# Kernel tuning notes

Measured on AMD Instinct MI355X. Metric: run time of the kernel, lower is better.

The kernel has to match this reference:

```python
import jax, jax.numpy as jnp
import numpy as np

EPS = 1e-7
C_CONST = 1.0


def gru_scan(x_seq, h0, Wih, Whh, bih, bhh):
    # x_seq: [T,B,E], h0: [B,H]; torch GRU gate order: r, z, n
    xg = jnp.einsum('tbe,ge->tbg', x_seq, Wih) + bih  # [T,B,3H]

    def step(h, xg_t):
        hg = h @ Whh.T + bhh
        xr, xz, xn = jnp.split(xg_t, 3, axis=-1)
        hr, hz, hn = jnp.split(hg, 3, axis=-1)
        r = jax.nn.sigmoid(xr + hr)
        z = jax.nn.sigmoid(xz + hz)
        n = jnp.tanh(xn + r * hn)
        h_new = (1.0 - z) * n + z * h
        return h_new, h_new

    hT, outs = jax.lax.scan(step, h0, xg)
    return outs, hT


def e2lorentz(x):
    # Euclidean -> Lorentz: [..., D] -> [..., D+1]
    rr = jnp.linalg.norm(x, axis=-1, keepdims=True)
    unit = x / rr
    return jnp.concatenate([unit * jnp.sinh(rr), jnp.cosh(rr)], axis=-1)


def arcosh(x):
    return jnp.log(x) + jnp.log1p(jnp.sqrt(x * x - 1.0 + EPS) / x)


def setup_inputs() -> dict:
    key = jax.random.key(0)
    ks = jax.random.split(key, 14)
    T, B, E, H, V = 64, 1024, 300, 256, 50000
    s = 0.05
    inp = {}
    inp['tokens'] = jax.random.randint(ks[0], (T, B), 0, V, dtype=jnp.int32)
    inp['hidden_state'] = jnp.zeros((2, B, H), jnp.float32)
    inp['emb'] = jax.random.normal(ks[1], (V, E), jnp.float32) * s
    inp['Wih_f'] = jax.random.normal(ks[2], (3 * H, E), jnp.float32) * s
    inp['Whh_f'] = jax.random.normal(ks[3], (3 * H, H), jnp.float32) * s
    inp['bih_f'] = jax.random.normal(ks[4], (3 * H,), jnp.float32) * s
    inp['bhh_f'] = jax.random.normal(ks[5], (3 * H,), jnp.float32) * s
    inp['Wih_b'] = jax.random.normal(ks[6], (3 * H, E), jnp.float32) * s
    inp['Whh_b'] = jax.random.normal(ks[7], (3 * H, H), jnp.float32) * s
    inp['bih_b'] = jax.random.normal(ks[8], (3 * H,), jnp.float32) * s
    inp['bhh_b'] = jax.random.normal(ks[9], (3 * H,), jnp.float32) * s
    inp['attn_W'] = jax.random.normal(ks[10], (2 * H, 2 * H), jnp.float32) * s
    inp['attn_b'] = jax.random.normal(ks[11], (2 * H,), jnp.float32) * s
    inp['centroid'] = jax.random.normal(ks[12], (2 * H,), jnp.float32) * s
    inp['beta'] = jax.random.normal(ks[13], (1,), jnp.float32) * s
    return inp


def reference(tokens, hidden_state, emb, Wih_f, Whh_f, bih_f, bhh_f,
              Wih_b, Whh_b, bih_b, bhh_b, attn_W, attn_b, centroid, beta):
    x = emb[tokens]  # [T,B,E]
    f_fwd, h_f = gru_scan(x, hidden_state[0], Wih_f, Whh_f, bih_f, bhh_f)
    f_bwd_rev, h_b = gru_scan(x[::-1], hidden_state[1], Wih_b, Whh_b, bih_b, bhh_b)
    f_bwd = f_bwd_rev[::-1]
    f_output = jnp.concatenate([f_fwd, f_bwd], axis=-1)  # [T,B,2H]
    h_output = jnp.stack([h_f, h_b], axis=0)             # [2,B,H]

    # hyperbolic attention scores
    a = jnp.tanh(jnp.einsum('tbd,od->tbo', f_output, attn_W) + attn_b)
    aL = e2lorentz(a)                      # [T,B,2H+1]
    uL = e2lorentz(centroid[None, None, :])  # [1,1,2H+1]
    m = aL * uL
    prod = jnp.clip(-jnp.sum(m[..., :-1], axis=-1) + m[..., -1], 1.0 + EPS, 1e16)
    dist = arcosh(prod)                    # [T,B]
    score = -beta[0] * dist - C_CONST
    score = score - score.max()
    alpha = jax.nn.softmax(score, axis=0)  # softmax over time

    # Klein-model features with Lorentz-factor (gamma) weighted midpoint
    fL = e2lorentz(f_output)
    fK = fL[..., :-1] / jnp.clip(fL[..., -1:], EPS, 1e16)  # [T,B,2H]
    dump = jnp.sqrt(jnp.clip(1.0 - jnp.sum(fK * fK, axis=-1), EPS, 1.0 - EPS))
    gamma = jnp.clip(1.0 / dump, 1.0 + EPS, 1e16)
    alpha = alpha * gamma
    alpha = alpha / jnp.sum(alpha, axis=0)
    out = jnp.sum(alpha[..., None] * fK, axis=0)[None]  # [1,B,2H]
    return out, h_output
```

## Files before the change

kernel.cpp:

```cpp
#include <hip/hip_runtime.h>
#include <hip/hip_bf16.h>
#include <math.h>

#define T_  64
#define B_  1024
#define E_  300
#define EP_ 320
#define H_  256
#define G3_ 768
#define D_  512
#define CH_ 16

typedef float f32x4 __attribute__((ext_vector_type(4)));
typedef short bf16x8 __attribute__((ext_vector_type(8)));
typedef unsigned short u16x4 __attribute__((ext_vector_type(4)));

__device__ __forceinline__ float bf2f(unsigned short u){ return __uint_as_float(((unsigned)u) << 16); }
__device__ __forceinline__ unsigned short f2bf(float x){
    __hip_bfloat16 h = __float2bfloat16(x);
    return *(unsigned short*)&h;
}
__device__ __forceinline__ float fsig(float x){ return 1.0f/(1.0f + __expf(-x)); }
__device__ __forceinline__ float ftanh(float x){ return 2.0f/(1.0f + __expf(-2.0f*x)) - 1.0f; }

__global__ void lorentz_u_kernel(const float* __restrict__ centroid,
                                 float* __restrict__ su)
{
    __shared__ float red[512];
    const int tid = threadIdx.x;
    float c = centroid[tid];
    red[tid] = c*c;
    __syncthreads();
    for (int s = 256; s > 0; s >>= 1){
        if (tid < s) red[tid] += red[tid + s];
        __syncthreads();
    }
    float rr = sqrtf(red[0]);
    su[tid] = c / rr * sinhf(rr);
    if (tid == 0) su[512] = coshf(rr);
}

__global__ void cast_pad_kernel(const float* __restrict__ src,
                                __hip_bfloat16* __restrict__ dst,
                                int ncols, int ncols_pad)
{
    long long r = blockIdx.x;
    int c = threadIdx.x;
    float v = (c < ncols) ? src[r*ncols + c] : 0.f;
    dst[r*ncols_pad + c] = __float2bfloat16(v);
}

__global__ void prep_bias_kernel(const float* __restrict__ bihf, const float* __restrict__ bhhf,
                                 const float* __restrict__ bihb, const float* __restrict__ bhhb,
                                 float* __restrict__ biasc)
{
    int c = threadIdx.x, d = blockIdx.x;
    const float* bih = d ? bihb : bihf;
    const float* bhh = d ? bhhb : bhhf;
    biasc[d*G3_ + c] = bih[c] + (c < 2*H_ ? bhh[c] : 0.f);
}

__global__ __launch_bounds__(256) void proj_kernel(
    const int* __restrict__ tokens, int tlo_f, int tlo_b,
    const __hip_bfloat16* __restrict__ embbf,
    const __hip_bfloat16* __restrict__ wihf, const __hip_bfloat16* __restrict__ wihb,
    const float* __restrict__ biasc,
    __hip_bfloat16* __restrict__ xgf, __hip_bfloat16* __restrict__ xgb)
{
    __shared__ char As[64 * 640];
    __shared__ char Ws[64 * 640];
    const int dir = blockIdx.z;
    const int tlo = dir ? tlo_b : tlo_f;
    const __hip_bfloat16* Wbf = dir ? wihb : wihf;
    const float* bias = biasc + dir*G3_;
    __hip_bfloat16* xg = dir ? xgb : xgf;
    const int* tok = tokens + (long long)tlo * B_;

    const int tid = threadIdx.x;
    const int n0 = blockIdx.x * 64;
    const int m0 = blockIdx.y * 64;

    {
        int row = tid >> 2, sub = tid & 3;
        long long tk = tok[m0 + row];
        const char* src = (const char*)(embbf + tk * EP_);
        char* dst = As + row * 640;
        int xm = (row & 7);
        #pragma unroll
        for (int j = 0; j < 10; ++j){
            int slot = sub + j*4;
            float4 v = *(const float4*)(src + slot*16);
            *(float4*)(dst + ((slot ^ xm) * 16)) = v;
        }
    }
    {
        #pragma unroll
        for (int it = 0; it < 10; ++it){
            int idx = it*256 + tid;
            int col = idx / 40, u = idx - col*40;
            float4 v = *(const float4*)(Wbf + (size_t)(n0 + col)*EP_ + u*8);
            *(float4*)(Ws + col*640 + ((u ^ (col & 7)) * 16)) = v;
        }
    }
    __syncthreads();

    const int lane = tid & 63, w = tid >> 6;
    const int arow = w*16 + (lane & 15);
    const int g = lane >> 4, l15 = lane & 15;
    const char* abase = As + arow * 640;
    const int amask = arow & 7;

    f32x4 acc[4];
    #pragma unroll
    for (int i = 0; i < 4; ++i) acc[i] = (f32x4){0.f,0.f,0.f,0.f};

    #pragma unroll
    for (int kc = 0; kc < 10; ++kc){
        int aslot = kc*4 + g;
        bf16x8 a = *(const bf16x8*)(abase + ((aslot ^ amask) * 16));
        #pragma unroll
        for (int ct = 0; ct < 4; ++ct){
            int cl = ct*16 + l15;
            bf16x8 b = *(const bf16x8*)(Ws + cl*640 + ((aslot ^ (cl & 7)) * 16));
            acc[ct] = __builtin_amdgcn_mfma_f32_16x16x32_bf16(a, b, acc[ct], 0, 0, 0);
        }
    }

    #pragma unroll
    for (int ct = 0; ct < 4; ++ct){
        int col = n0 + ct*16 + l15;
        float bv = bias[col];
        int rbase = m0 + w*16 + g*4;
        #pragma unroll
        for (int i = 0; i < 4; ++i)
            xg[(long long)(rbase + i)*G3_ + col] = __float2bfloat16(acc[ct][i] + bv);
    }
}

__global__ __launch_bounds__(512, 1) void gru_chunk_kernel(
    const __hip_bfloat16* __restrict__ xg_f, const __hip_bfloat16* __restrict__ xg_b,
    int tlo_f, int tlo_b,
    __hip_bfloat16* __restrict__ f_bf,
    float* __restrict__ hf32g,
    const float* __restrict__ hidden,
    const __hip_bfloat16* __restrict__ whhbf,
    const float* __restrict__ bhh_f, const float* __restrict__ bhh_b,
    float* __restrict__ hout, int s0)
{
    __shared__ char hlds[2][16 * 512];
    __shared__ char xlds[2][16 * 1536];
    __shared__ float blds[256];
    const int bid = blockIdx.x;
    const int dir = bid & 1;
    const int b0 = (bid >> 1) * 16;
    const int tid = threadIdx.x;
    const int lane = tid & 63, w = tid >> 6;
    const int g = lane >> 4, l15 = lane & 15;
    const int jq = w*32 + g*4;

    const __hip_bfloat16* xg = dir ? xg_b : xg_f;
    const int tlo = dir ? tlo_b : tlo_f;
    const float* bhh = dir ? bhh_b : bhh_f;
    const __hip_bfloat16* Wb = whhbf + (size_t)dir * G3_ * H_;
    float* hfg = hf32g + (size_t)dir * B_ * H_;
    const int b = b0 + l15;

    bf16x8 Wf[3][2][8];
    #pragma unroll
    for (int gate = 0; gate < 3; ++gate)
        #pragma unroll
        for (int tl = 0; tl < 2; ++tl)
            #pragma unroll
            for (int kc = 0; kc < 8; ++kc)
                Wf[gate][tl][kc] = *(const bf16x8*)(Wb +
                    ((size_t)(gate*H_ + w*32 + tl*16 + l15))*H_ + kc*32 + g*8);

    if (tid < 256) blds[tid] = bhh[2*H_ + tid];

    const float* hsrc = (s0 == 0 ? hidden : hf32g) + (size_t)dir * B_ * H_;
    #pragma unroll
    for (int it = 0; it < 2; ++it){
        int idx = it*512 + tid;
        int r = idx >> 6, q = idx & 63;
        float4 v = *(const float4*)(hsrc + ((size_t)(b0 + r))*H_ + q*4);
        unsigned short t4[4] = { f2bf(v.x), f2bf(v.y), f2bf(v.z), f2bf(v.w) };
        *(uint2*)(hlds[0] + r*512 + (((q>>1) ^ (r&7))*16) + (q&1)*8) = *(uint2*)t4;
    }
    f32x4 carry[2];
    #pragma unroll
    for (int tl = 0; tl < 2; ++tl)
        carry[tl] = *(const f32x4*)&hsrc[(size_t)b*H_ + jq + tl*16];

    auto stage_x = [&](char* dst, const __hip_bfloat16* xgt){
        #pragma unroll
        for (int i = 0; i < 3; ++i){
            int U = (i*8 + w)*64 + lane;
            int r = U / 96;
            int sbase = U - r*96;
            int usrc = sbase - r; if (usrc < 0) usrc += 96;
            const char* src = (const char*)xgt + (size_t)(b0 + r)*1536 + usrc*16;
            __builtin_amdgcn_global_load_lds(
                (const __attribute__((address_space(1))) void*)src,
                (__attribute__((address_space(3))) void*)(dst + (i*8 + w)*1024),
                16, 0, 0);
        }
    };
    {
        const int t0 = dir ? (63 - s0) : s0;
        stage_x(xlds[0], xg + (size_t)(t0 - tlo)*B_*G3_);
    }
    __syncthreads();

    int cur = 0, hc = 0;
    for (int s = s0; s < s0 + CH_; ++s){
        const int t = dir ? (63 - s) : s;

        if (s < s0 + CH_ - 1){
            const int tn = dir ? (t - 1) : (t + 1);
            stage_x(xlds[cur ^ 1], xg + (size_t)(tn - tlo)*B_*G3_);
        }

        f32x4 acc[3][2];
        #pragma unroll
        for (int gate = 0; gate < 3; ++gate)
            #pragma unroll
            for (int tl = 0; tl < 2; ++tl)
                acc[gate][tl] = (f32x4){0.f,0.f,0.f,0.f};

        {
            bf16x8 hb[4];
            #pragma unroll
            for (int kc = 0; kc < 4; ++kc)
                hb[kc] = *(const bf16x8*)(hlds[hc] + l15*512 + (((kc*4 + g) ^ (l15&7))*16));
            #pragma unroll
            for (int kc = 0; kc < 4; ++kc)
                #pragma unroll
                for (int gate = 0; gate < 3; ++gate)
                    #pragma unroll
                    for (int tl = 0; tl < 2; ++tl)
                        acc[gate][tl] = __builtin_amdgcn_mfma_f32_16x16x32_bf16(
                            Wf[gate][tl][kc], hb[kc], acc[gate][tl], 0, 0, 0);
        }
        {
            bf16x8 hb[4];
            #pragma unroll
            for (int kc = 0; kc < 4; ++kc)
                hb[kc] = *(const bf16x8*)(hlds[hc] + l15*512 + ((((kc+4)*4 + g) ^ (l15&7))*16));
            #pragma unroll
            for (int kc = 0; kc < 4; ++kc)
                #pragma unroll
                for (int gate = 0; gate < 3; ++gate)
                    #pragma unroll
                    for (int tl = 0; tl < 2; ++tl)
                        acc[gate][tl] = __builtin_amdgcn_mfma_f32_16x16x32_bf16(
                            Wf[gate][tl][kc+4], hb[kc], acc[gate][tl], 0, 0, 0);
        }

        #pragma unroll
        for (int tl = 0; tl < 2; ++tl){
            u16x4 xv[3];
            #pragma unroll
            for (int gate = 0; gate < 3; ++gate){
                int u = gate*32 + w*4 + tl*2 + (g >> 1);
                int sl = u + l15; if (sl >= 96) sl -= 96;
                xv[gate] = *(const u16x4*)(xlds[cur] + l15*1536 + sl*16 + (g & 1)*8);
            }
            f32x4 bhn = *(const f32x4*)&blds[jq + tl*16];

            unsigned short hb4[4];
            float hn4[4];
            #pragma unroll
            for (int i = 0; i < 4; ++i){
                float xr = bf2f(xv[0][i]);
                float xz = bf2f(xv[1][i]);
                float xn = bf2f(xv[2][i]);
                float r_ = fsig(xr + acc[0][tl][i]);
                float z_ = fsig(xz + acc[1][tl][i]);
                float n_ = ftanh(xn + r_*(acc[2][tl][i] + bhn[i]));
                float hnew = (1.f - z_)*n_ + z_*carry[tl][i];
                carry[tl][i] = hnew;
                hn4[i] = hnew;
                hb4[i] = f2bf(hnew);
            }
            int j0 = jq + tl*16;
            int slot = j0 >> 3;
            *(uint2*)(hlds[hc^1] + l15*512 + ((slot ^ (l15&7))*16) + (j0&7)*2) = *(uint2*)hb4;
            *(u16x4*)((char*)f_bf + (((size_t)t*B_ + b)*D_ + dir*H_ + j0)*2) = *(u16x4*)hb4;
            if (s == 63)
                *(float4*)&hout[(size_t)dir*B_*H_ + (size_t)b*H_ + j0] = *(float4*)hn4;
        }

        __syncthreads();
        cur ^= 1; hc ^= 1;
    }

    #pragma unroll
    for (int tl = 0; tl < 2; ++tl)
        *(f32x4*)&hfg[(size_t)b*H_ + jq + tl*16] = carry[tl];
}

__global__ __launch_bounds__(256) void attn_score_kernel(
    const __hip_bfloat16* __restrict__ f_bf, const __hip_bfloat16* __restrict__ Wbf,
    const float* __restrict__ attn_b, const float* __restrict__ su,
    const float* __restrict__ beta, float* __restrict__ score,
    float* __restrict__ rr2)
{
    __shared__ char WL[65536];
    const int tid = threadIdx.x;
    const int lane = tid & 63, w = tid >> 6;
    const int g = lane >> 4, l15 = lane & 15;
    const long long m0 = (long long)blockIdx.x * 64;
    const long long arow = m0 + w*16 + l15;

    bf16x8 a[16];
    const __hip_bfloat16* ap = f_bf + arow*D_;
    #pragma unroll
    for (int kc = 0; kc < 16; ++kc)
        a[kc] = *(const bf16x8*)(ap + kc*32 + g*8);

    {
        float s2 = 0.f;
        #pragma unroll
        for (int kc = 0; kc < 16; ++kc){
            const unsigned short* hb = (const unsigned short*)&a[kc];
            #pragma unroll
            for (int q = 0; q < 8; ++q){ float x = bf2f(hb[q]); s2 += x*x; }
        }
        s2 += __shfl_xor(s2, 16);
        s2 += __shfl_xor(s2, 32);
        if (g == 0) rr2[arow] = s2;
    }

    float pdot[4] = {0,0,0,0}, pa2[4] = {0,0,0,0};

    for (int nc = 0; nc < 8; ++nc){
        {
            const __hip_bfloat16* wsrc = Wbf + (size_t)nc*64*D_;
            #pragma unroll
            for (int it = 0; it < 16; ++it){
                int idx = it*256 + tid;
                int cl = idx >> 6, jj = idx & 63;
                float4 v = *(const float4*)(wsrc + (size_t)cl*D_ + jj*8);
                *(float4*)(WL + (cl*64 + (jj ^ (cl & 7)))*16) = v;
            }
        }
        __syncthreads();

        f32x4 acc[4];
        #pragma unroll
        for (int i = 0; i < 4; ++i) acc[i] = (f32x4){0.f,0.f,0.f,0.f};
        #pragma unroll
        for (int kc = 0; kc < 16; ++kc){
            #pragma unroll
            for (int ct = 0; ct < 4; ++ct){
                int cl = ct*16 + l15;
                bf16x8 b = *(const bf16x8*)(WL + (cl*64 + ((kc*4 + g) ^ (l15 & 7)))*16);
                acc[ct] = __builtin_amdgcn_mfma_f32_16x16x32_bf16(a[kc], b, acc[ct], 0, 0, 0);
            }
        }
        __syncthreads();

        #pragma unroll
        for (int ct = 0; ct < 4; ++ct){
            int col = nc*64 + ct*16 + l15;
            float bc = attn_b[col], sc = su[col];
            #pragma unroll
            for (int i = 0; i < 4; ++i){
                float av = ftanh(acc[ct][i] + bc);
                pdot[i] += av*sc;
                pa2[i]  += av*av;
            }
        }
    }

    #pragma unroll
    for (int m = 1; m < 16; m <<= 1){
        #pragma unroll
        for (int i = 0; i < 4; ++i){
            pdot[i] += __shfl_xor(pdot[i], m);
            pa2[i]  += __shfl_xor(pa2[i],  m);
        }
    }
    if (l15 == 0){
        const float cu = su[512], bb = beta[0];
        #pragma unroll
        for (int i = 0; i < 4; ++i){
            long long row = m0 + w*16 + g*4 + i;
            float ra  = sqrtf(pa2[i]);
            float shc = sinhf(ra)/ra;
            float prod = cu*coshf(ra) - shc*pdot[i];
            prod = fminf(fmaxf(prod, 1.0f + 1e-7f), 1e16f);
            float dist = logf(prod) + log1pf(sqrtf(prod*prod - 1.0f + 1e-7f)/prod);
            score[row] = -bb * dist;
        }
    }
}

__global__ __launch_bounds__(256) void pool_kernel(
    const __hip_bfloat16* __restrict__ f_bf, const float* __restrict__ score,
    const float* __restrict__ rr2, float* __restrict__ out)
{
    __shared__ float wss[64];
    const int tid = threadIdx.x;
    const long long b = blockIdx.x;

    if (tid < 64){
        int t = tid;
        float sc = score[t*B_ + b];
        float mx = sc;
        #pragma unroll
        for (int m = 1; m < 64; m <<= 1) mx = fmaxf(mx, __shfl_xor(mx, m));
        float e = expf(sc - mx);
        float rr = sqrtf(rr2[t*B_ + b]);
        float th = tanhf(rr);
        float omt = 1.0f - th*th;
        omt = fminf(fmaxf(omt, 1e-7f), 1.0f - 1e-7f);
        float gamma = 1.0f / sqrtf(omt);
        gamma = fminf(fmaxf(gamma, 1.0f + 1e-7f), 1e16f);
        float wgt = e * gamma;
        float ssum = wgt;
        #pragma unroll
        for (int m = 1; m < 64; m <<= 1) ssum += __shfl_xor(ssum, m);
        wss[t] = (wgt / ssum) * (th / rr);
    }
    __syncthreads();

    #pragma unroll
    for (int dd = 0; dd < 2; ++dd){
        int d = tid + dd*256;
        float acc = 0.f;
        for (int t = 0; t < 64; ++t)
            acc += wss[t] * __bfloat162float(f_bf[((long long)t*B_ + b)*D_ + d]);
        out[b*D_ + d] = acc;
    }
}

extern "C" void kernel_launch(void* const* d_in, const int* in_sizes, int n_in,
                              void* d_out, int out_size, void* d_ws, size_t ws_size,
                              hipStream_t stream)
{
    const int*   tokens = (const int*)  d_in[0];
    const float* hidden = (const float*)d_in[1];
    const float* emb    = (const float*)d_in[2];
    const float* Wih_f  = (const float*)d_in[3];
    const float* Whh_f  = (const float*)d_in[4];
    const float* bih_f  = (const float*)d_in[5];
    const float* bhh_f  = (const float*)d_in[6];
    const float* Wih_b  = (const float*)d_in[7];
    const float* Whh_b  = (const float*)d_in[8];
    const float* bih_b  = (const float*)d_in[9];
    const float* bhh_b  = (const float*)d_in[10];
    const float* attn_W = (const float*)d_in[11];
    const float* attn_b = (const float*)d_in[12];
    const float* centroid = (const float*)d_in[13];
    const float* beta   = (const float*)d_in[14];

    const int V = in_sizes[2] / E_;

    char* w = (char*)d_ws;
    __hip_bfloat16* f_bf  = (__hip_bfloat16*)w;  w += (size_t)T_*B_*D_*2;
    __hip_bfloat16* xg_f  = (__hip_bfloat16*)w;  w += (size_t)CH_*B_*G3_*2;
    __hip_bfloat16* xg_b  = (__hip_bfloat16*)w;  w += (size_t)CH_*B_*G3_*2;
    float*          hf32g = (float*)w;           w += (size_t)2*B_*H_*4;
    __hip_bfloat16* embbf = (__hip_bfloat16*)w;  w += (size_t)V*EP_*2;
    __hip_bfloat16* wihf  = (__hip_bfloat16*)w;  w += (size_t)G3_*EP_*2;
    __hip_bfloat16* wihb  = (__hip_bfloat16*)w;  w += (size_t)G3_*EP_*2;
    __hip_bfloat16* whhbf = (__hip_bfloat16*)w;  w += (size_t)2*G3_*H_*2;
    __hip_bfloat16* wat   = (__hip_bfloat16*)w;  w += (size_t)D_*D_*2;
    float*          biasc = (float*)w;           w += (size_t)2*G3_*4;
    float*          score = (float*)w;           w += (size_t)T_*B_*4;
    float*          rr2   = (float*)w;           w += (size_t)T_*B_*4;
    float*          su    = (float*)w;           w += 513*4;

    float* out  = (float*)d_out;
    float* hout = out + (long long)B_*D_;

    lorentz_u_kernel<<<1, 512, 0, stream>>>(centroid, su);
    prep_bias_kernel<<<2, G3_, 0, stream>>>(bih_f, bhh_f, bih_b, bhh_b, biasc);
    cast_pad_kernel<<<V,   EP_, 0, stream>>>(emb,    embbf, E_, EP_);
    cast_pad_kernel<<<G3_, EP_, 0, stream>>>(Wih_f,  wihf,  E_, EP_);
    cast_pad_kernel<<<G3_, EP_, 0, stream>>>(Wih_b,  wihb,  E_, EP_);
    cast_pad_kernel<<<G3_, H_,  0, stream>>>(Whh_f,  whhbf,            H_, H_);
    cast_pad_kernel<<<G3_, H_,  0, stream>>>(Whh_b,  whhbf + (size_t)G3_*H_, H_, H_);
    cast_pad_kernel<<<D_,  D_,  0, stream>>>(attn_W, wat,   D_, D_);

    for (int c = 0; c < T_/CH_; ++c){
        int tlo_f = c*CH_;
        int tlo_b = (T_ - CH_) - c*CH_;
        int s0 = c*CH_;
        proj_kernel<<<dim3(12, CH_*16, 2), 256, 0, stream>>>(
            tokens, tlo_f, tlo_b, embbf, wihf, wihb, biasc, xg_f, xg_b);
        gru_chunk_kernel<<<128, 512, 0, stream>>>(
            xg_f, xg_b, tlo_f, tlo_b, f_bf, hf32g, hidden,
            whhbf, bhh_f, bhh_b, hout, s0);
    }

    attn_score_kernel<<<1024, 256, 0, stream>>>(f_bf, wat, attn_b, su, beta, score, rr2);
    pool_kernel<<<1024, 256, 0, stream>>>(f_bf, score, rr2, out);
}
```

Before: 687.4 us.

## Reuse weight tiles across row tiles and batch f_bf stores in pairs

proj_kernel now keeps its Wih tile in LDS and loops over four 64-row token tiles per block, so W is loaded a quarter as often and the grid shrinks. attn_score_kernel processes 128 rows per block with two A register sets sharing each B fragment, halving attn_W staging. gru_chunk_kernel buffers its per-step f_bf output and writes two timesteps together on odd steps. The cost is more registers and longer serial work per block, which lowers parallelism.

Measured after the change: 705.4 us. 2.6% more time.

```diff
diff --git a/kernel.cpp b/kernel.cpp
--- a/kernel.cpp
+++ b/kernel.cpp
@@ -78,21 +78,7 @@
 
     const int tid = threadIdx.x;
     const int n0 = blockIdx.x * 64;
-    const int m0 = blockIdx.y * 64;
-
-    {
-        int row = tid >> 2, sub = tid & 3;
-        long long tk = tok[m0 + row];
-        const char* src = (const char*)(embbf + tk * EP_);
-        char* dst = As + row * 640;
-        int xm = (row & 7);
-        #pragma unroll
-        for (int j = 0; j < 10; ++j){
-            int slot = sub + j*4;
-            float4 v = *(const float4*)(src + slot*16);
-            *(float4*)(dst + ((slot ^ xm) * 16)) = v;
-        }
-    }
+
     {
         #pragma unroll
         for (int it = 0; it < 10; ++it){
@@ -102,38 +88,56 @@
             *(float4*)(Ws + col*640 + ((u ^ (col & 7)) * 16)) = v;
         }
     }
-    __syncthreads();
 
     const int lane = tid & 63, w = tid >> 6;
-    const int arow = w*16 + (lane & 15);
     const int g = lane >> 4, l15 = lane & 15;
+    const int arow = w*16 + l15;
     const char* abase = As + arow * 640;
     const int amask = arow & 7;
 
-    f32x4 acc[4];
-    #pragma unroll
-    for (int i = 0; i < 4; ++i) acc[i] = (f32x4){0.f,0.f,0.f,0.f};
-
-    #pragma unroll
-    for (int kc = 0; kc < 10; ++kc){
-        int aslot = kc*4 + g;
-        bf16x8 a = *(const bf16x8*)(abase + ((aslot ^ amask) * 16));
+    for (int rt = 0; rt < 4; ++rt){
+        const int m0 = (blockIdx.y*4 + rt) * 64;
+        {
+            int row = tid >> 2, sub = tid & 3;
+            long long tk = tok[m0 + row];
+            const char* src = (const char*)(embbf + tk * EP_);
+            char* dst = As + row * 640;
+            int xm = (row & 7);
+            #pragma unroll
+            for (int j = 0; j < 10; ++j){
+                int slot = sub + j*4;
+                float4 v = *(const float4*)(src + slot*16);
+                *(float4*)(dst + ((slot ^ xm) * 16)) = v;
+            }
+        }
+        __syncthreads();
+
+        f32x4 acc[4];
+        #pragma unroll
+        for (int i = 0; i < 4; ++i) acc[i] = (f32x4){0.f,0.f,0.f,0.f};
+
+        #pragma unroll
+        for (int kc = 0; kc < 10; ++kc){
+            int aslot = kc*4 + g;
+            bf16x8 a = *(const bf16x8*)(abase + ((aslot ^ amask) * 16));
+            #pragma unroll
+            for (int ct = 0; ct < 4; ++ct){
+                int cl = ct*16 + l15;
+                bf16x8 b = *(const bf16x8*)(Ws + cl*640 + ((aslot ^ (cl & 7)) * 16));
+                acc[ct] = __builtin_amdgcn_mfma_f32_16x16x32_bf16(a, b, acc[ct], 0, 0, 0);
+            }
+        }
+
         #pragma unroll
         for (int ct = 0; ct < 4; ++ct){
-            int cl = ct*16 + l15;
-            bf16x8 b = *(const bf16x8*)(Ws + cl*640 + ((aslot ^ (cl & 7)) * 16));
-            acc[ct] = __builtin_amdgcn_mfma_f32_16x16x32_bf16(a, b, acc[ct], 0, 0, 0);
-        }
-    }
-
-    #pragma unroll
-    for (int ct = 0; ct < 4; ++ct){
-        int col = n0 + ct*16 + l15;
-        float bv = bias[col];
-        int rbase = m0 + w*16 + g*4;
-        #pragma unroll
-        for (int i = 0; i < 4; ++i)
-            xg[(long long)(rbase + i)*G3_ + col] = __float2bfloat16(acc[ct][i] + bv);
+            int col = n0 + ct*16 + l15;
+            float bv = bias[col];
+            int rbase = m0 + w*16 + g*4;
+            #pragma unroll
+            for (int i = 0; i < 4; ++i)
+                xg[(long long)(rbase + i)*G3_ + col] = __float2bfloat16(acc[ct][i] + bv);
+        }
+        __syncthreads();
     }
 }
 
@@ -212,6 +216,8 @@
     __syncthreads();
 
     int cur = 0, hc = 0;
+    u16x4 pend[2];
+    int t_pend = -1;
     for (int s = s0; s < s0 + CH_; ++s){
         const int t = dir ? (63 - s) : s;
 
@@ -256,6 +262,7 @@
                             Wf[gate][tl][kc+4], hb[kc], acc[gate][tl], 0, 0, 0);
         }
 
+        u16x4 outv[2];
         #pragma unroll
         for (int tl = 0; tl < 2; ++tl){
             u16x4 xv[3];
@@ -285,9 +292,24 @@
             int j0 = jq + tl*16;
             int slot = j0 >> 3;
             *(uint2*)(hlds[hc^1] + l15*512 + ((slot ^ (l15&7))*16) + (j0&7)*2) = *(uint2*)hb4;
-            *(u16x4*)((char*)f_bf + (((size_t)t*B_ + b)*D_ + dir*H_ + j0)*2) = *(u16x4*)hb4;
+            outv[tl] = *(u16x4*)hb4;
             if (s == 63)
                 *(float4*)&hout[(size_t)dir*B_*H_ + (size_t)b*H_ + j0] = *(float4*)hn4;
+        }
+
+        if (s & 1){
+            if (t_pend >= 0){
+                #pragma unroll
+                for (int tl = 0; tl < 2; ++tl)
+                    *(u16x4*)((char*)f_bf + (((size_t)t_pend*B_ + b)*D_ + dir*H_ + jq + tl*16)*2) = pend[tl];
+            }
+            #pragma unroll
+            for (int tl = 0; tl < 2; ++tl)
+                *(u16x4*)((char*)f_bf + (((size_t)t*B_ + b)*D_ + dir*H_ + jq + tl*16)*2) = outv[tl];
+            t_pend = -1;
+        } else {
+            pend[0] = outv[0]; pend[1] = outv[1];
+            t_pend = t;
         }
 
         __syncthreads();
@@ -309,29 +331,32 @@
     const int tid = threadIdx.x;
     const int lane = tid & 63, w = tid >> 6;
     const int g = lane >> 4, l15 = lane & 15;
-    const long long m0 = (long long)blockIdx.x * 64;
-    const long long arow = m0 + w*16 + l15;
-
-    bf16x8 a[16];
-    const __hip_bfloat16* ap = f_bf + arow*D_;
-    #pragma unroll
-    for (int kc = 0; kc < 16; ++kc)
-        a[kc] = *(const bf16x8*)(ap + kc*32 + g*8);
-
-    {
+    const long long m0 = (long long)blockIdx.x * 128;
+
+    bf16x8 a[2][16];
+    #pragma unroll
+    for (int rg = 0; rg < 2; ++rg){
+        const __hip_bfloat16* ap = f_bf + (m0 + rg*64 + w*16 + l15)*D_;
+        #pragma unroll
+        for (int kc = 0; kc < 16; ++kc)
+            a[rg][kc] = *(const bf16x8*)(ap + kc*32 + g*8);
+    }
+
+    #pragma unroll
+    for (int rg = 0; rg < 2; ++rg){
         float s2 = 0.f;
         #pragma unroll
         for (int kc = 0; kc < 16; ++kc){
-            const unsigned short* hb = (const unsigned short*)&a[kc];
+            const unsigned short* hb = (const unsigned short*)&a[rg][kc];
             #pragma unroll
             for (int q = 0; q < 8; ++q){ float x = bf2f(hb[q]); s2 += x*x; }
         }
         s2 += __shfl_xor(s2, 16);
         s2 += __shfl_xor(s2, 32);
-        if (g == 0) rr2[arow] = s2;
-    }
-
-    float pdot[4] = {0,0,0,0}, pa2[4] = {0,0,0,0};
+        if (g == 0) rr2[m0 + rg*64 + w*16 + l15] = s2;
+    }
+
+    float pdot[2][4] = {}, pa2[2][4] = {};
 
     for (int nc = 0; nc < 8; ++nc){
         {
@@ -346,16 +371,19 @@
         }
         __syncthreads();
 
-        f32x4 acc[4];
-        #pragma unroll
-        for (int i = 0; i < 4; ++i) acc[i] = (f32x4){0.f,0.f,0.f,0.f};
+        f32x4 acc[2][4];
+        #pragma unroll
+        for (int rg = 0; rg < 2; ++rg)
+            #pragma unroll
+            for (int i = 0; i < 4; ++i) acc[rg][i] = (f32x4){0.f,0.f,0.f,0.f};
         #pragma unroll
         for (int kc = 0; kc < 16; ++kc){
             #pragma unroll
             for (int ct = 0; ct < 4; ++ct){
                 int cl = ct*16 + l15;
-                bf16x8 b = *(const bf16x8*)(WL + (cl*64 + ((kc*4 + g) ^ (l15 & 7)))*16);
-                acc[ct] = __builtin_amdgcn_mfma_f32_16x16x32_bf16(a[kc], b, acc[ct], 0, 0, 0);
+                bf16x8 bfr = *(const bf16x8*)(WL + (cl*64 + ((kc*4 + g) ^ (l15 & 7)))*16);
+                acc[0][ct] = __builtin_amdgcn_mfma_f32_16x16x32_bf16(a[0][kc], bfr, acc[0][ct], 0, 0, 0);
+                acc[1][ct] = __builtin_amdgcn_mfma_f32_16x16x32_bf16(a[1][kc], bfr, acc[1][ct], 0, 0, 0);
             }
         }
         __syncthreads();
@@ -365,33 +393,41 @@
             int col = nc*64 + ct*16 + l15;
             float bc = attn_b[col], sc = su[col];
             #pragma unroll
+            for (int rg = 0; rg < 2; ++rg){
+                #pragma unroll
+                for (int i = 0; i < 4; ++i){
+                    float av = ftanh(acc[rg][ct][i] + bc);
+                    pdot[rg][i] += av*sc;
+                    pa2[rg][i]  += av*av;
+                }
+            }
+        }
+    }
+
+    #pragma unroll
+    for (int m = 1; m < 16; m <<= 1){
+        #pragma unroll
+        for (int rg = 0; rg < 2; ++rg)
+            #pragma unroll
             for (int i = 0; i < 4; ++i){
-                float av = ftanh(acc[ct][i] + bc);
-                pdot[i] += av*sc;
-                pa2[i]  += av*av;
-            }
-        }
-    }
-
-    #pragma unroll
-    for (int m = 1; m < 16; m <<= 1){
-        #pragma unroll
-        for (int i = 0; i < 4; ++i){
-            pdot[i] += __shfl_xor(pdot[i], m);
-            pa2[i]  += __shfl_xor(pa2[i],  m);
-        }
+                pdot[rg][i] += __shfl_xor(pdot[rg][i], m);
+                pa2[rg][i]  += __shfl_xor(pa2[rg][i],  m);
+            }
     }
     if (l15 == 0){
         const float cu = su[512], bb = beta[0];
         #pragma unroll
-        for (int i = 0; i < 4; ++i){
-            long long row = m0 + w*16 + g*4 + i;
-            float ra  = sqrtf(pa2[i]);
-            float shc = sinhf(ra)/ra;
-            float prod = cu*coshf(ra) - shc*pdot[i];
-            prod = fminf(fmaxf(prod, 1.0f + 1e-7f), 1e16f);
-            float dist = logf(prod) + log1pf(sqrtf(prod*prod - 1.0f + 1e-7f)/prod);
-            score[row] = -bb * dist;
+        for (int rg = 0; rg < 2; ++rg){
+            #pragma unroll
+            for (int i = 0; i < 4; ++i){
+                long long row = m0 + rg*64 + w*16 + g*4 + i;
+                float ra  = sqrtf(pa2[rg][i]);
+                float shc = sinhf(ra)/ra;
+                float prod = cu*coshf(ra) - shc*pdot[rg][i];
+                prod = fminf(fmaxf(prod, 1.0f + 1e-7f), 1e16f);
+                float dist = logf(prod) + log1pf(sqrtf(prod*prod - 1.0f + 1e-7f)/prod);
+                score[row] = -bb * dist;
+            }
         }
     }
 }
@@ -488,13 +524,13 @@
         int tlo_f = c*CH_;
         int tlo_b = (T_ - CH_) - c*CH_;
         int s0 = c*CH_;
-        proj_kernel<<<dim3(12, CH_*16, 2), 256, 0, stream>>>(
+        proj_kernel<<<dim3(12, 64, 2), 256, 0, stream>>>(
             tokens, tlo_f, tlo_b, embbf, wihf, wihb, biasc, xg_f, xg_b);
         gru_chunk_kernel<<<128, 512, 0, stream>>>(
             xg_f, xg_b, tlo_f, tlo_b, f_bf, hf32g, hidden,
             whhbf, bhh_f, bhh_b, hout, s0);
     }
 
-    attn_score_kernel<<<1024, 256, 0, stream>>>(f_bf, wat, attn_b, su, beta, score, rr2);
+    attn_score_kernel<<<512, 256, 0, stream>>>(f_bf, wat, attn_b, su, beta, score, rr2);
     pool_kernel<<<1024, 256, 0, stream>>>(f_bf, score, rr2, out);
 }
```

## Reuse W tiles across row tiles, batch GRU output stores, double-buffer attention weights

Applied to the files above, without the earlier changes.

The input-projection kernel now keeps each W tile in shared memory and loops over four row tiles per block, cutting redundant weight loads and the grid size fourfold. The GRU chunk kernel holds each step's bf16 outputs in registers and writes two timesteps at once on odd steps, thinning global stores inside the recurrent loop. The attention-score kernel splits the weights into 32-column chunks, stages them with async global_load_lds into a double buffer with a rotated layout, and overlaps the next chunk's load with the current MFMA work. Each block now does more serial work, with more barriers.

Result: faster. 620.0 us (-9.8%).

```diff
diff --git a/kernel.cpp b/kernel.cpp
--- a/kernel.cpp
+++ b/kernel.cpp
@@ -78,21 +78,7 @@
 
     const int tid = threadIdx.x;
     const int n0 = blockIdx.x * 64;
-    const int m0 = blockIdx.y * 64;
-
-    {
-        int row = tid >> 2, sub = tid & 3;
-        long long tk = tok[m0 + row];
-        const char* src = (const char*)(embbf + tk * EP_);
-        char* dst = As + row * 640;
-        int xm = (row & 7);
-        #pragma unroll
-        for (int j = 0; j < 10; ++j){
-            int slot = sub + j*4;
-            float4 v = *(const float4*)(src + slot*16);
-            *(float4*)(dst + ((slot ^ xm) * 16)) = v;
-        }
-    }
+
     {
         #pragma unroll
         for (int it = 0; it < 10; ++it){
@@ -102,38 +88,56 @@
             *(float4*)(Ws + col*640 + ((u ^ (col & 7)) * 16)) = v;
         }
     }
-    __syncthreads();
 
     const int lane = tid & 63, w = tid >> 6;
-    const int arow = w*16 + (lane & 15);
     const int g = lane >> 4, l15 = lane & 15;
+    const int arow = w*16 + l15;
     const char* abase = As + arow * 640;
     const int amask = arow & 7;
 
-    f32x4 acc[4];
-    #pragma unroll
-    for (int i = 0; i < 4; ++i) acc[i] = (f32x4){0.f,0.f,0.f,0.f};
-
-    #pragma unroll
-    for (int kc = 0; kc < 10; ++kc){
-        int aslot = kc*4 + g;
-        bf16x8 a = *(const bf16x8*)(abase + ((aslot ^ amask) * 16));
+    for (int rt = 0; rt < 4; ++rt){
+        const int m0 = (blockIdx.y*4 + rt) * 64;
+        {
+            int row = tid >> 2, sub = tid & 3;
+            long long tk = tok[m0 + row];
+            const char* src = (const char*)(embbf + tk * EP_);
+            char* dst = As + row * 640;
+            int xm = (row & 7);
+            #pragma unroll
+            for (int j = 0; j < 10; ++j){
+                int slot = sub + j*4;
+                float4 v = *(const float4*)(src + slot*16);
+                *(float4*)(dst + ((slot ^ xm) * 16)) = v;
+            }
+        }
+        __syncthreads();
+
+        f32x4 acc[4];
+        #pragma unroll
+        for (int i = 0; i < 4; ++i) acc[i] = (f32x4){0.f,0.f,0.f,0.f};
+
+        #pragma unroll
+        for (int kc = 0; kc < 10; ++kc){
+            int aslot = kc*4 + g;
+            bf16x8 a = *(const bf16x8*)(abase + ((aslot ^ amask) * 16));
+            #pragma unroll
+            for (int ct = 0; ct < 4; ++ct){
+                int cl = ct*16 + l15;
+                bf16x8 b = *(const bf16x8*)(Ws + cl*640 + ((aslot ^ (cl & 7)) * 16));
+                acc[ct] = __builtin_amdgcn_mfma_f32_16x16x32_bf16(a, b, acc[ct], 0, 0, 0);
+            }
+        }
+
         #pragma unroll
         for (int ct = 0; ct < 4; ++ct){
-            int cl = ct*16 + l15;
-            bf16x8 b = *(const bf16x8*)(Ws + cl*640 + ((aslot ^ (cl & 7)) * 16));
-            acc[ct] = __builtin_amdgcn_mfma_f32_16x16x32_bf16(a, b, acc[ct], 0, 0, 0);
-        }
-    }
-
-    #pragma unroll
-    for (int ct = 0; ct < 4; ++ct){
-        int col = n0 + ct*16 + l15;
-        float bv = bias[col];
-        int rbase = m0 + w*16 + g*4;
-        #pragma unroll
-        for (int i = 0; i < 4; ++i)
-            xg[(long long)(rbase + i)*G3_ + col] = __float2bfloat16(acc[ct][i] + bv);
+            int col = n0 + ct*16 + l15;
+            float bv = bias[col];
+            int rbase = m0 + w*16 + g*4;
+            #pragma unroll
+            for (int i = 0; i < 4; ++i)
+                xg[(long long)(rbase + i)*G3_ + col] = __float2bfloat16(acc[ct][i] + bv);
+        }
+        __syncthreads();
     }
 }
 
@@ -212,6 +216,8 @@
     __syncthreads();
 
     int cur = 0, hc = 0;
+    u16x4 pend[2];
+    int t_pend = -1;
     for (int s = s0; s < s0 + CH_; ++s){
         const int t = dir ? (63 - s) : s;
 
@@ -256,6 +262,7 @@
                             Wf[gate][tl][kc+4], hb[kc], acc[gate][tl], 0, 0, 0);
         }
 
+        u16x4 outv[2];
         #pragma unroll
         for (int tl = 0; tl < 2; ++tl){
             u16x4 xv[3];
@@ -285,9 +292,24 @@
             int j0 = jq + tl*16;
             int slot = j0 >> 3;
             *(uint2*)(hlds[hc^1] + l15*512 + ((slot ^ (l15&7))*16) + (j0&7)*2) = *(uint2*)hb4;
-            *(u16x4*)((char*)f_bf + (((size_t)t*B_ + b)*D_ + dir*H_ + j0)*2) = *(u16x4*)hb4;
+            outv[tl] = *(u16x4*)hb4;
             if (s == 63)
                 *(float4*)&hout[(size_t)dir*B_*H_ + (size_t)b*H_ + j0] = *(float4*)hn4;
+        }
+
+        if (s & 1){
+            if (t_pend >= 0){
+                #pragma unroll
+                for (int tl = 0; tl < 2; ++tl)
+                    *(u16x4*)((char*)f_bf + (((size_t)t_pend*B_ + b)*D_ + dir*H_ + jq + tl*16)*2) = pend[tl];
+            }
+            #pragma unroll
+            for (int tl = 0; tl < 2; ++tl)
+                *(u16x4*)((char*)f_bf + (((size_t)t*B_ + b)*D_ + dir*H_ + jq + tl*16)*2) = outv[tl];
+            t_pend = -1;
+        } else {
+            pend[0] = outv[0]; pend[1] = outv[1];
+            t_pend = t;
         }
 
         __syncthreads();
@@ -305,7 +327,7 @@
     const float* __restrict__ beta, float* __restrict__ score,
     float* __restrict__ rr2)
 {
-    __shared__ char WL[65536];
+    __shared__ char WL[2][32 * 1024];
     const int tid = threadIdx.x;
     const int lane = tid & 63, w = tid >> 6;
     const int g = lane >> 4, l15 = lane & 15;
@@ -331,38 +353,47 @@
         if (g == 0) rr2[arow] = s2;
     }
 
+    auto stage_w = [&](char* dst, int nc){
+        const __hip_bfloat16* wsrc = Wbf + (size_t)nc*32*D_;
+        #pragma unroll
+        for (int i = 0; i < 8; ++i){
+            int U = i*256 + tid;
+            int r = U >> 6, sl = U & 63;
+            int usrc = (sl - r) & 63;
+            const char* src = (const char*)(wsrc + (size_t)r*D_) + usrc*16;
+            __builtin_amdgcn_global_load_lds(
+                (const __attribute__((address_space(1))) void*)src,
+                (__attribute__((address_space(3))) void*)(dst + U*16),
+                16, 0, 0);
+        }
+    };
+
+    stage_w(WL[0], 0);
+    __syncthreads();
+
     float pdot[4] = {0,0,0,0}, pa2[4] = {0,0,0,0};
-
-    for (int nc = 0; nc < 8; ++nc){
-        {
-            const __hip_bfloat16* wsrc = Wbf + (size_t)nc*64*D_;
-            #pragma unroll
-            for (int it = 0; it < 16; ++it){
-                int idx = it*256 + tid;
-                int cl = idx >> 6, jj = idx & 63;
-                float4 v = *(const float4*)(wsrc + (size_t)cl*D_ + jj*8);
-                *(float4*)(WL + (cl*64 + (jj ^ (cl & 7)))*16) = v;
-            }
-        }
-        __syncthreads();
-
-        f32x4 acc[4];
-        #pragma unroll
-        for (int i = 0; i < 4; ++i) acc[i] = (f32x4){0.f,0.f,0.f,0.f};
+    int cur = 0;
+
+    for (int nc = 0; nc < 16; ++nc){
+        if (nc < 15) stage_w(WL[cur ^ 1], nc + 1);
+
+        f32x4 acc[2];
+        acc[0] = (f32x4){0.f,0.f,0.f,0.f};
+        acc[1] = (f32x4){0.f,0.f,0.f,0.f};
         #pragma unroll
         for (int kc = 0; kc < 16; ++kc){
-            #pragma unroll
-            for (int ct = 0; ct < 4; ++ct){
+            int u = kc*4 + g;
+            #pragma unroll
+            for (int ct = 0; ct < 2; ++ct){
                 int cl = ct*16 + l15;
-                bf16x8 b = *(const bf16x8*)(WL + (cl*64 + ((kc*4 + g) ^ (l15 & 7)))*16);
-                acc[ct] = __builtin_amdgcn_mfma_f32_16x16x32_bf16(a[kc], b, acc[ct], 0, 0, 0);
-            }
-        }
-        __syncthreads();
-
-        #pragma unroll
-        for (int ct = 0; ct < 4; ++ct){
-            int col = nc*64 + ct*16 + l15;
+                bf16x8 bfr = *(const bf16x8*)(WL[cur] + cl*1024 + (((u + cl) & 63)*16));
+                acc[ct] = __builtin_amdgcn_mfma_f32_16x16x32_bf16(a[kc], bfr, acc[ct], 0, 0, 0);
+            }
+        }
+
+        #pragma unroll
+        for (int ct = 0; ct < 2; ++ct){
+            int col = nc*32 + ct*16 + l15;
             float bc = attn_b[col], sc = su[col];
             #pragma unroll
             for (int i = 0; i < 4; ++i){
@@ -371,6 +402,9 @@
                 pa2[i]  += av*av;
             }
         }
+
+        __syncthreads();
+        cur ^= 1;
     }
 
     #pragma unroll
@@ -488,7 +522,7 @@
         int tlo_f = c*CH_;
         int tlo_b = (T_ - CH_) - c*CH_;
         int s0 = c*CH_;
-        proj_kernel<<<dim3(12, CH_*16, 2), 256, 0, stream>>>(
+        proj_kernel<<<dim3(12, 64, 2), 256, 0, stream>>>(
             tokens, tlo_f, tlo_b, embbf, wihf, wihb, biasc, xg_f, xg_b);
         gru_chunk_kernel<<<128, 512, 0, stream>>>(
             xg_f, xg_b, tlo_f, tlo_b, f_bf, hf32g, hidden,
```
